# Kernel optimization log

Measured on AMD Instinct MI355X. Metric: run time of the kernel, lower is better.

The kernel has to match this reference:

```python
import jax, jax.numpy as jnp
import numpy as np
import math

NUM_HEADS = 8
QUERY_SIZE = 256
QK_SIZE = QUERY_SIZE // NUM_HEADS  # 32
VO_SIZE = QUERY_SIZE // NUM_HEADS  # 32
SEQ = 4096


def setup_inputs() -> dict:
    key = jax.random.key(0)
    kq, kk, kv, km, kwq, kwk, kwv, kwo = jax.random.split(key, 8)
    # equinox Linear weight shape is (out_features, in_features); y = W @ x
    lim_in = 1.0 / math.sqrt(QUERY_SIZE)
    lim_hd = 1.0 / math.sqrt(NUM_HEADS * VO_SIZE)
    return {
        "query": jax.random.normal(kq, (SEQ, QUERY_SIZE), dtype=jnp.float32),
        "key_": jax.random.normal(kk, (SEQ, QUERY_SIZE), dtype=jnp.float32),
        "value": jax.random.normal(kv, (SEQ, QUERY_SIZE), dtype=jnp.float32),
        "radial_mask": jax.random.uniform(km, (SEQ,), dtype=jnp.float32),
        "Wq": jax.random.uniform(kwq, (NUM_HEADS * QK_SIZE, QUERY_SIZE), minval=-lim_in, maxval=lim_in, dtype=jnp.float32),
        "Wk": jax.random.uniform(kwk, (NUM_HEADS * QK_SIZE, QUERY_SIZE), minval=-lim_in, maxval=lim_in, dtype=jnp.float32),
        "Wv": jax.random.uniform(kwv, (NUM_HEADS * VO_SIZE, QUERY_SIZE), minval=-lim_in, maxval=lim_in, dtype=jnp.float32),
        "Wo": jax.random.uniform(kwo, (QUERY_SIZE, NUM_HEADS * VO_SIZE), minval=-lim_hd, maxval=lim_hd, dtype=jnp.float32),
    }


def reference(query, key_, value, radial_mask, Wq, Wk, Wv, Wo):
    S = query.shape[0]
    # QKV projections, split into heads: [S, H, D]
    q = (query @ Wq.T).reshape(S, NUM_HEADS, QK_SIZE)
    k = (key_ @ Wk.T).reshape(S, NUM_HEADS, QK_SIZE)
    v = (value @ Wv.T).reshape(S, NUM_HEADS, VO_SIZE)
    # radial scaling of values (per kv position)
    v = radial_mask[:, None, None] * v
    # scaled dot-product attention per head; logits: [H, S, S]
    scale = 1.0 / math.sqrt(QK_SIZE)
    logits = jnp.einsum("shd,Shd->hsS", q * scale, k)
    weights = jax.nn.softmax(logits, axis=-1)
    attn = jnp.einsum("hsS,Shd->shd", weights, v).reshape(S, NUM_HEADS * VO_SIZE)
    # output projection
    return attn @ Wo.T
```

## Files before the change

kernel.cpp:

```cpp
#include <hip/hip_runtime.h>
#include <cstdint>

#define SEQ 4096
#define NH 8
#define DH 32

typedef __bf16 bf16x8 __attribute__((ext_vector_type(8)));
typedef float f32x4 __attribute__((ext_vector_type(4)));
typedef float f32x8 __attribute__((ext_vector_type(8)));
typedef float f32x16 __attribute__((ext_vector_type(16)));
typedef unsigned short u16x8 __attribute__((ext_vector_type(8)));
typedef unsigned u32x4 __attribute__((ext_vector_type(4)));
typedef unsigned u32x2 __attribute__((ext_vector_type(2)));
typedef int i32x2 __attribute__((ext_vector_type(2)));

#define MFMA16 __builtin_amdgcn_mfma_f32_16x16x32_bf16
#define MFMA32 __builtin_amdgcn_mfma_f32_32x32x16_bf16

#define QSCALE 0.25503902427f

__device__ inline bf16x8 ld_bf8(const unsigned short* p) {
    return __builtin_bit_cast(bf16x8, *(const u16x8*)p);
}
__device__ inline unsigned short bfbits(float v) {
    return __builtin_bit_cast(unsigned short, (__bf16)v);
}
__device__ inline bf16x8 cvt_f8(f32x8 v) {
    bf16x8 r;
#pragma unroll
    for (int i = 0; i < 8; i++) r[i] = (__bf16)v[i];
    return r;
}
__device__ inline unsigned cvtpk(float lo, float hi) {
    unsigned r;
    asm("v_cvt_pk_bf16_f32 %0, %1, %2" : "=v"(r) : "v"(lo), "v"(hi));
    return r;
}

__global__ __launch_bounds__(256) void precvt_kernel(
    const float* __restrict__ x0, const float* __restrict__ x1, const float* __restrict__ x2,
    const float* __restrict__ w0, const float* __restrict__ w1, const float* __restrict__ w2,
    const float* __restrict__ w3,
    unsigned short* __restrict__ bx0, unsigned short* __restrict__ bx1,
    unsigned short* __restrict__ bx2, unsigned short* __restrict__ bw0,
    unsigned short* __restrict__ bw1, unsigned short* __restrict__ bw2,
    unsigned short* __restrict__ bw3) {
    const int i = blockIdx.x * 256 + threadIdx.x;
    const float* src;
    unsigned short* dst;
    int off;
    float scale = 1.0f;
    if (i < 393216) {
        const int sel = i >> 17;
        off = i & 131071;
        src = (sel == 0) ? x0 : (sel == 1) ? x1 : x2;
        dst = (sel == 0) ? bx0 : (sel == 1) ? bx1 : bx2;
        if (sel == 0) scale = QSCALE;
    } else {
        const int j = i - 393216;
        const int sel = j >> 13;
        off = j & 8191;
        src = (sel == 0) ? w0 : (sel == 1) ? w1 : (sel == 2) ? w2 : w3;
        dst = (sel == 0) ? bw0 : (sel == 1) ? bw1 : (sel == 2) ? bw2 : bw3;
    }
    f32x8 v = ((const f32x8*)src)[off];
    u16x8 r;
#pragma unroll
    for (int j = 0; j < 8; j++) r[j] = bfbits(v[j] * scale);
    ((u16x8*)dst)[off] = r;
}

__global__ __launch_bounds__(256, 4) void proj_bf16_kernel(
    const unsigned short* __restrict__ X0, const unsigned short* __restrict__ X1,
    const unsigned short* __restrict__ X2, const unsigned short* __restrict__ W0,
    const unsigned short* __restrict__ W1, const unsigned short* __restrict__ W2,
    const float* __restrict__ radial,
    unsigned short* __restrict__ outq, unsigned short* __restrict__ outk,
    unsigned short* __restrict__ outv) {
    const int sel = blockIdx.y;
    const unsigned short* X = (sel == 0) ? X0 : (sel == 1) ? X1 : X2;
    const unsigned short* W = (sel == 0) ? W0 : (sel == 1) ? W1 : W2;
    const int lane = threadIdx.x & 63;
    const int w = threadIdx.x >> 6;
    const int cl = lane & 15;
    const int h4 = lane >> 4;
    const int t = blockIdx.x * 4 + w;
    const int m0 = (t >> 3) * 32;
    const int n0 = (t & 7) * 32;

    const unsigned short* xa0 = X + (m0 + cl) * 256 + h4 * 8;
    const unsigned short* xa1 = xa0 + 16 * 256;
    const unsigned short* wb0 = W + (n0 + cl) * 256 + h4 * 8;
    const unsigned short* wb1 = wb0 + 16 * 256;

    f32x4 acc00 = {0.f, 0.f, 0.f, 0.f}, acc01 = {0.f, 0.f, 0.f, 0.f};
    f32x4 acc10 = {0.f, 0.f, 0.f, 0.f}, acc11 = {0.f, 0.f, 0.f, 0.f};
#pragma unroll
    for (int ksi = 0; ksi < 8; ksi++) {
        bf16x8 a0 = ld_bf8(xa0 + ksi * 32);
        bf16x8 a1 = ld_bf8(xa1 + ksi * 32);
        bf16x8 b0 = ld_bf8(wb0 + ksi * 32);
        bf16x8 b1 = ld_bf8(wb1 + ksi * 32);
        acc00 = MFMA16(a0, b0, acc00, 0, 0, 0);
        acc01 = MFMA16(a0, b1, acc01, 0, 0, 0);
        acc10 = MFMA16(a1, b0, acc10, 0, 0, 0);
        acc11 = MFMA16(a1, b1, acc11, 0, 0, 0);
    }

#pragma unroll
    for (int am = 0; am < 2; am++) {
#pragma unroll
        for (int r = 0; r < 4; r++) {
            const int cm = m0 + am * 16 + h4 * 4 + r;
            float rm = (sel == 2) ? radial[cm] : 0.f;
#pragma unroll
            for (int bn = 0; bn < 2; bn++) {
                float v = am ? (bn ? acc11[r] : acc10[r]) : (bn ? acc01[r] : acc00[r]);
                const int cn = n0 + bn * 16 + cl;
                const int h = cn >> 5, d = cn & 31;
                if (sel == 0) outq[(h * SEQ + cm) * DH + d] = bfbits(v);
                else if (sel == 1) outk[(h * SEQ + cm) * DH + d] = bfbits(v);
                else outv[(h * DH + d) * SEQ + cm] = bfbits(v * rm);
            }
        }
    }
}

__global__ __launch_bounds__(256) void proj_f32_kernel(
    const float* __restrict__ X0, const float* __restrict__ X1, const float* __restrict__ X2,
    const float* __restrict__ W0, const float* __restrict__ W1, const float* __restrict__ W2,
    const float* __restrict__ radial,
    unsigned short* __restrict__ outq, unsigned short* __restrict__ outk,
    unsigned short* __restrict__ outv) {
    const int sel = blockIdx.y;
    const float* X = (sel == 0) ? X0 : (sel == 1) ? X1 : X2;
    const float* W = (sel == 0) ? W0 : (sel == 1) ? W1 : W2;
    const int lane = threadIdx.x & 63;
    const int w = threadIdx.x >> 6;
    const int cl = lane & 15;
    const int h4 = lane >> 4;
    const int t = blockIdx.x * 4 + w;
    const int m0 = (t >> 3) * 32;
    const int n0 = (t & 7) * 32;

    const float* xa0 = X + (m0 + cl) * 256 + h4 * 8;
    const float* xa1 = xa0 + 16 * 256;
    const float* wb0 = W + (n0 + cl) * 256 + h4 * 8;
    const float* wb1 = wb0 + 16 * 256;

    f32x4 acc00 = {0.f, 0.f, 0.f, 0.f}, acc01 = {0.f, 0.f, 0.f, 0.f};
    f32x4 acc10 = {0.f, 0.f, 0.f, 0.f}, acc11 = {0.f, 0.f, 0.f, 0.f};
#pragma unroll
    for (int ksi = 0; ksi < 8; ksi++) {
        bf16x8 a0 = cvt_f8(*(const f32x8*)(xa0 + ksi * 32));
        bf16x8 a1 = cvt_f8(*(const f32x8*)(xa1 + ksi * 32));
        bf16x8 b0 = cvt_f8(*(const f32x8*)(wb0 + ksi * 32));
        bf16x8 b1 = cvt_f8(*(const f32x8*)(wb1 + ksi * 32));
        acc00 = MFMA16(a0, b0, acc00, 0, 0, 0);
        acc01 = MFMA16(a0, b1, acc01, 0, 0, 0);
        acc10 = MFMA16(a1, b0, acc10, 0, 0, 0);
        acc11 = MFMA16(a1, b1, acc11, 0, 0, 0);
    }
#pragma unroll
    for (int am = 0; am < 2; am++) {
#pragma unroll
        for (int r = 0; r < 4; r++) {
            const int cm = m0 + am * 16 + h4 * 4 + r;
            float rm = (sel == 2) ? radial[cm] : 0.f;
#pragma unroll
            for (int bn = 0; bn < 2; bn++) {
                float v = am ? (bn ? acc11[r] : acc10[r]) : (bn ? acc01[r] : acc00[r]);
                const int cn = n0 + bn * 16 + cl;
                const int h = cn >> 5, d = cn & 31;
                if (sel == 0) outq[(h * SEQ + cm) * DH + d] = bfbits(v * QSCALE);
                else if (sel == 1) outk[(h * SEQ + cm) * DH + d] = bfbits(v);
                else outv[(h * DH + d) * SEQ + cm] = bfbits(v * rm);
            }
        }
    }
}

__device__ inline f32x16 qk_step(bf16x8 kf0, bf16x8 kf1, const bf16x8& qf0,
                                 const bf16x8& qf1) {
    f32x16 s = {0.f, 0.f, 0.f, 0.f, 0.f, 0.f, 0.f, 0.f,
                0.f, 0.f, 0.f, 0.f, 0.f, 0.f, 0.f, 0.f};
    __builtin_amdgcn_s_setprio(1);
    s = MFMA32(kf0, qf0, s, 0, 0, 0);
    s = MFMA32(kf1, qf1, s, 0, 0, 0);
    __builtin_amdgcn_s_setprio(0);
    return s;
}

__device__ inline void sm_pv_step(const f32x16& s, bf16x8 vt0, bf16x8 vt1,
                                  f32x16& oacc, float& ls) {
    float p[16];
#pragma unroll
    for (int r = 0; r < 16; r++) p[r] = __builtin_amdgcn_exp2f(s[r]);
    {
        float s01 = p[0] + p[1], s23 = p[2] + p[3], s45 = p[4] + p[5], s67 = p[6] + p[7];
        float s89 = p[8] + p[9], sab = p[10] + p[11], scd = p[12] + p[13], sef = p[14] + p[15];
        ls += ((s01 + s23) + (s45 + s67)) + ((s89 + sab) + (scd + sef));
    }
    unsigned a01 = cvtpk(p[0], p[1]), a23 = cvtpk(p[2], p[3]);
    unsigned a45 = cvtpk(p[4], p[5]), a67 = cvtpk(p[6], p[7]);
    i32x2 r0 = __builtin_amdgcn_permlane32_swap((int)a01, (int)a45, false, false);
    i32x2 r1 = __builtin_amdgcn_permlane32_swap((int)a23, (int)a67, false, false);
    u32x4 pb0w = {(unsigned)r0[0], (unsigned)r1[0], (unsigned)r0[1], (unsigned)r1[1]};
    unsigned a89 = cvtpk(p[8], p[9]), aab = cvtpk(p[10], p[11]);
    unsigned acd = cvtpk(p[12], p[13]), aef = cvtpk(p[14], p[15]);
    i32x2 r2 = __builtin_amdgcn_permlane32_swap((int)a89, (int)acd, false, false);
    i32x2 r3 = __builtin_amdgcn_permlane32_swap((int)aab, (int)aef, false, false);
    u32x4 pb1w = {(unsigned)r2[0], (unsigned)r3[0], (unsigned)r2[1], (unsigned)r3[1]};
    __builtin_amdgcn_s_setprio(1);
    oacc = MFMA32(vt0, __builtin_bit_cast(bf16x8, pb0w), oacc, 0, 0, 0);
    oacc = MFMA32(vt1, __builtin_bit_cast(bf16x8, pb1w), oacc, 0, 0, 0);
    __builtin_amdgcn_s_setprio(0);
}

__global__ __launch_bounds__(512, 2) void attn_kernel(
    const unsigned short* __restrict__ Q, const unsigned short* __restrict__ K,
    const unsigned short* __restrict__ Vt, unsigned short* __restrict__ An) {
    __shared__ float cO[7][64][16];
    __shared__ float cls[7][4][32];
    const int lane = threadIdx.x & 63;
    const int w = threadIdx.x >> 6;
    const int l31 = lane & 31;
    const int hi = lane >> 5;

    int bid = blockIdx.x;
    bid = (bid & 7) * 32 + (bid >> 3);
    const int head = bid >> 5;
    const int m0 = (bid & 31) * 128;

    const unsigned short* qh = Q + head * (SEQ * DH);
    const unsigned short* kh = K + head * (SEQ * DH);
    const unsigned short* vh = Vt + head * (DH * SEQ);

    bf16x8 q0[4], q1[4];
#pragma unroll
    for (int c = 0; c < 4; c++) {
        q0[c] = ld_bf8(qh + (m0 + c * 32 + l31) * DH + hi * 8);
        q1[c] = ld_bf8(qh + (m0 + c * 32 + l31) * DH + 16 + hi * 8);
    }

    f32x16 o[4];
    float ls[4];
#pragma unroll
    for (int c = 0; c < 4; c++) {
        o[c] = (f32x16){0.f, 0.f, 0.f, 0.f, 0.f, 0.f, 0.f, 0.f,
                        0.f, 0.f, 0.f, 0.f, 0.f, 0.f, 0.f, 0.f};
        ls[c] = 0.f;
    }

    const unsigned short* kp = kh + (w * 512 + l31) * DH + hi * 8;
    const unsigned short* vp = vh + l31 * SEQ + w * 512 + hi * 8;

    for (int nb = 0; nb < 16; nb++) {
        bf16x8 kc0 = ld_bf8(kp), kc1 = ld_bf8(kp + 16);
        bf16x8 vc0 = ld_bf8(vp), vc1 = ld_bf8(vp + 16);
#pragma unroll
        for (int c = 0; c < 4; c++) {
            f32x16 s = qk_step(kc0, kc1, q0[c], q1[c]);
            sm_pv_step(s, vc0, vc1, o[c], ls[c]);
        }
        kp += 32 * DH;
        vp += 32;
    }

#pragma unroll
    for (int c = 0; c < 4; c++) ls[c] += __shfl_xor(ls[c], 32);

#pragma unroll
    for (int c = 0; c < 4; c++) {
        if (w > 0) {
#pragma unroll
            for (int i = 0; i < 16; i++) cO[w - 1][lane][i] = o[c][i];
            if (hi == 0) cls[w - 1][c][l31] = ls[c];
        }
        __syncthreads();
        if (w == 0) {
#pragma unroll
            for (int j = 0; j < 7; j++) {
#pragma unroll
                for (int i = 0; i < 16; i++) o[c][i] += cO[j][lane][i];
            }
        }
        __syncthreads();
    }

    if (w == 0) {
#pragma unroll
        for (int c = 0; c < 4; c++) {
            float lt = ls[c];
#pragma unroll
            for (int j = 0; j < 7; j++) lt += cls[j][c][l31];
            const float inv = 1.0f / lt;
            unsigned short* op = An + (m0 + c * 32 + l31) * 256 + head * DH;
#pragma unroll
            for (int g = 0; g < 4; g++) {
                unsigned lo = cvtpk(o[c][4 * g] * inv, o[c][4 * g + 1] * inv);
                unsigned hw = cvtpk(o[c][4 * g + 2] * inv, o[c][4 * g + 3] * inv);
                *(u32x2*)(op + 8 * g + 4 * hi) = (u32x2){lo, hw};
            }
        }
    }
}

__global__ __launch_bounds__(256, 4) void oproj_bf16_kernel(
    const unsigned short* __restrict__ An, const unsigned short* __restrict__ Wo,
    float* __restrict__ out) {
    const int lane = threadIdx.x & 63;
    const int w = threadIdx.x >> 6;
    const int cl = lane & 15;
    const int h4 = lane >> 4;
    const int t = blockIdx.x * 4 + w;
    const int m0 = (t >> 4) * 32;
    const int n0 = (t & 15) * 16;

    const unsigned short* ap0 = An + (m0 + cl) * 256 + h4 * 8;
    const unsigned short* ap1 = ap0 + 16 * 256;
    const unsigned short* wb0 = Wo + (n0 + cl) * 256 + h4 * 8;

    f32x4 acc00 = {0.f, 0.f, 0.f, 0.f}, acc10 = {0.f, 0.f, 0.f, 0.f};
#pragma unroll
    for (int ksi = 0; ksi < 8; ksi++) {
        bf16x8 a0 = ld_bf8(ap0 + ksi * 32);
        bf16x8 a1 = ld_bf8(ap1 + ksi * 32);
        bf16x8 b0 = ld_bf8(wb0 + ksi * 32);
        acc00 = MFMA16(a0, b0, acc00, 0, 0, 0);
        acc10 = MFMA16(a1, b0, acc10, 0, 0, 0);
    }
#pragma unroll
    for (int am = 0; am < 2; am++) {
#pragma unroll
        for (int r = 0; r < 4; r++) {
            const int cm = m0 + am * 16 + h4 * 4 + r;
            out[cm * 256 + n0 + cl] = am ? acc10[r] : acc00[r];
        }
    }
}

__global__ __launch_bounds__(256) void oproj_f32_kernel(
    const unsigned short* __restrict__ An, const float* __restrict__ Wo,
    float* __restrict__ out) {
    const int lane = threadIdx.x & 63;
    const int w = threadIdx.x >> 6;
    const int cl = lane & 15;
    const int h4 = lane >> 4;
    const int t = blockIdx.x * 4 + w;
    const int m0 = (t >> 3) * 32;
    const int n0 = (t & 7) * 32;

    const unsigned short* ap0 = An + (m0 + cl) * 256 + h4 * 8;
    const unsigned short* ap1 = ap0 + 16 * 256;
    const float* wb0 = Wo + (n0 + cl) * 256 + h4 * 8;
    const float* wb1 = wb0 + 16 * 256;

    f32x4 acc00 = {0.f, 0.f, 0.f, 0.f}, acc01 = {0.f, 0.f, 0.f, 0.f};
    f32x4 acc10 = {0.f, 0.f, 0.f, 0.f}, acc11 = {0.f, 0.f, 0.f, 0.f};
#pragma unroll
    for (int ksi = 0; ksi < 8; ksi++) {
        bf16x8 a0 = ld_bf8(ap0 + ksi * 32);
        bf16x8 a1 = ld_bf8(ap1 + ksi * 32);
        bf16x8 b0 = cvt_f8(*(const f32x8*)(wb0 + ksi * 32));
        bf16x8 b1 = cvt_f8(*(const f32x8*)(wb1 + ksi * 32));
        acc00 = MFMA16(a0, b0, acc00, 0, 0, 0);
        acc01 = MFMA16(a0, b1, acc01, 0, 0, 0);
        acc10 = MFMA16(a1, b0, acc10, 0, 0, 0);
        acc11 = MFMA16(a1, b1, acc11, 0, 0, 0);
    }
#pragma unroll
    for (int am = 0; am < 2; am++) {
#pragma unroll
        for (int r = 0; r < 4; r++) {
            const int cm = m0 + am * 16 + h4 * 4 + r;
#pragma unroll
            for (int bn = 0; bn < 2; bn++) {
                float v = am ? (bn ? acc11[r] : acc10[r]) : (bn ? acc01[r] : acc00[r]);
                out[cm * 256 + n0 + bn * 16 + cl] = v;
            }
        }
    }
}

extern "C" void kernel_launch(void* const* d_in, const int* in_sizes, int n_in,
                              void* d_out, int out_size, void* d_ws, size_t ws_size,
                              hipStream_t stream) {
    const float* query = (const float*)d_in[0];
    const float* key_ = (const float*)d_in[1];
    const float* value = (const float*)d_in[2];
    const float* radial = (const float*)d_in[3];
    const float* Wq = (const float*)d_in[4];
    const float* Wk = (const float*)d_in[5];
    const float* Wv = (const float*)d_in[6];
    const float* Wo = (const float*)d_in[7];

    const size_t MB = 1u << 20;
    uint8_t* base = (uint8_t*)d_ws;
    unsigned short* wq = (unsigned short*)(base + 0 * MB);
    unsigned short* wk = (unsigned short*)(base + 2 * MB);
    unsigned short* wv = (unsigned short*)(base + 4 * MB);
    unsigned short* wa = (unsigned short*)(base + 6 * MB);

    if (ws_size >= (size_t)(15.5 * 1024 * 1024)) {
        unsigned short* bX0 = (unsigned short*)(base + 8 * MB);
        unsigned short* bX1 = (unsigned short*)(base + 10 * MB);
        unsigned short* bX2 = (unsigned short*)(base + 12 * MB);
        unsigned short* bWq = (unsigned short*)(base + 14 * MB);
        unsigned short* bWk = (unsigned short*)(base + 14 * MB + 128 * 1024);
        unsigned short* bWv = (unsigned short*)(base + 14 * MB + 256 * 1024);
        unsigned short* bWo = (unsigned short*)(base + 14 * MB + 384 * 1024);
        precvt_kernel<<<1664, 256, 0, stream>>>(query, key_, value, Wq, Wk, Wv, Wo,
                                                bX0, bX1, bX2, bWq, bWk, bWv, bWo);
        proj_bf16_kernel<<<dim3(256, 3), 256, 0, stream>>>(bX0, bX1, bX2, bWq, bWk, bWv,
                                                           radial, wq, wk, wv);
        attn_kernel<<<256, 512, 0, stream>>>(wq, wk, wv, wa);
        oproj_bf16_kernel<<<512, 256, 0, stream>>>(wa, bWo, (float*)d_out);
    } else {
        proj_f32_kernel<<<dim3(256, 3), 256, 0, stream>>>(query, key_, value, Wq, Wk, Wv,
                                                          radial, wq, wk, wv);
        attn_kernel<<<256, 512, 0, stream>>>(wq, wk, wv, wa);
        oproj_f32_kernel<<<256, 256, 0, stream>>>(wa, Wo, (float*)d_out);
    }
}
```

Before: 62.18 us.

## Swap MFMA operands for V projection to coalesce transposed stores; drop setprio

For the V projection, the MFMA operands are swapped so each lane's accumulator rows run along head dimension d and columns along sequence. Stores into the transposed Vt layout then write contiguous sequence positions across lanes instead of scattered 2-byte writes. The radial mask is loaded once per lane rather than per element. Separately, the s_setprio raise and lower around the MFMA pairs in the attention inner loop is removed, which changes wave scheduling priority and could help or hurt the overlap of matrix and softmax work.

New measurement: 61.67 us. No clear change (-0.8%).

```diff
diff --git a/kernel.cpp b/kernel.cpp
--- a/kernel.cpp
+++ b/kernel.cpp
@@ -95,32 +95,59 @@
 
     f32x4 acc00 = {0.f, 0.f, 0.f, 0.f}, acc01 = {0.f, 0.f, 0.f, 0.f};
     f32x4 acc10 = {0.f, 0.f, 0.f, 0.f}, acc11 = {0.f, 0.f, 0.f, 0.f};
-#pragma unroll
-    for (int ksi = 0; ksi < 8; ksi++) {
-        bf16x8 a0 = ld_bf8(xa0 + ksi * 32);
-        bf16x8 a1 = ld_bf8(xa1 + ksi * 32);
-        bf16x8 b0 = ld_bf8(wb0 + ksi * 32);
-        bf16x8 b1 = ld_bf8(wb1 + ksi * 32);
-        acc00 = MFMA16(a0, b0, acc00, 0, 0, 0);
-        acc01 = MFMA16(a0, b1, acc01, 0, 0, 0);
-        acc10 = MFMA16(a1, b0, acc10, 0, 0, 0);
-        acc11 = MFMA16(a1, b1, acc11, 0, 0, 0);
-    }
-
-#pragma unroll
-    for (int am = 0; am < 2; am++) {
-#pragma unroll
-        for (int r = 0; r < 4; r++) {
-            const int cm = m0 + am * 16 + h4 * 4 + r;
-            float rm = (sel == 2) ? radial[cm] : 0.f;
-#pragma unroll
-            for (int bn = 0; bn < 2; bn++) {
-                float v = am ? (bn ? acc11[r] : acc10[r]) : (bn ? acc01[r] : acc00[r]);
-                const int cn = n0 + bn * 16 + cl;
-                const int h = cn >> 5, d = cn & 31;
-                if (sel == 0) outq[(h * SEQ + cm) * DH + d] = bfbits(v);
-                else if (sel == 1) outk[(h * SEQ + cm) * DH + d] = bfbits(v);
-                else outv[(h * DH + d) * SEQ + cm] = bfbits(v * rm);
+
+    if (sel < 2) {
+#pragma unroll
+        for (int ksi = 0; ksi < 8; ksi++) {
+            bf16x8 a0 = ld_bf8(xa0 + ksi * 32);
+            bf16x8 a1 = ld_bf8(xa1 + ksi * 32);
+            bf16x8 b0 = ld_bf8(wb0 + ksi * 32);
+            bf16x8 b1 = ld_bf8(wb1 + ksi * 32);
+            acc00 = MFMA16(a0, b0, acc00, 0, 0, 0);
+            acc01 = MFMA16(a0, b1, acc01, 0, 0, 0);
+            acc10 = MFMA16(a1, b0, acc10, 0, 0, 0);
+            acc11 = MFMA16(a1, b1, acc11, 0, 0, 0);
+        }
+        unsigned short* out = (sel == 0) ? outq : outk;
+#pragma unroll
+        for (int am = 0; am < 2; am++) {
+#pragma unroll
+            for (int r = 0; r < 4; r++) {
+                const int cm = m0 + am * 16 + h4 * 4 + r;
+#pragma unroll
+                for (int bn = 0; bn < 2; bn++) {
+                    float v = am ? (bn ? acc11[r] : acc10[r]) : (bn ? acc01[r] : acc00[r]);
+                    const int cn = n0 + bn * 16 + cl;
+                    const int h = cn >> 5, d = cn & 31;
+                    out[(h * SEQ + cm) * DH + d] = bfbits(v);
+                }
+            }
+        }
+    } else {
+#pragma unroll
+        for (int ksi = 0; ksi < 8; ksi++) {
+            bf16x8 a0 = ld_bf8(xa0 + ksi * 32);
+            bf16x8 a1 = ld_bf8(xa1 + ksi * 32);
+            bf16x8 b0 = ld_bf8(wb0 + ksi * 32);
+            bf16x8 b1 = ld_bf8(wb1 + ksi * 32);
+            acc00 = MFMA16(b0, a0, acc00, 0, 0, 0);
+            acc01 = MFMA16(b0, a1, acc01, 0, 0, 0);
+            acc10 = MFMA16(b1, a0, acc10, 0, 0, 0);
+            acc11 = MFMA16(b1, a1, acc11, 0, 0, 0);
+        }
+        const int h = n0 >> 5;
+        const float rm0 = radial[m0 + cl];
+        const float rm1 = radial[m0 + 16 + cl];
+#pragma unroll
+        for (int wb = 0; wb < 2; wb++) {
+#pragma unroll
+            for (int r = 0; r < 4; r++) {
+                const int d = wb * 16 + h4 * 4 + r;
+                unsigned short* vrow = outv + (h * DH + d) * SEQ + m0;
+                float v0 = wb ? acc10[r] : acc00[r];
+                float v1 = wb ? acc11[r] : acc01[r];
+                vrow[cl] = bfbits(v0 * rm0);
+                vrow[16 + cl] = bfbits(v1 * rm1);
             }
         }
     }
@@ -150,31 +177,59 @@
 
     f32x4 acc00 = {0.f, 0.f, 0.f, 0.f}, acc01 = {0.f, 0.f, 0.f, 0.f};
     f32x4 acc10 = {0.f, 0.f, 0.f, 0.f}, acc11 = {0.f, 0.f, 0.f, 0.f};
-#pragma unroll
-    for (int ksi = 0; ksi < 8; ksi++) {
-        bf16x8 a0 = cvt_f8(*(const f32x8*)(xa0 + ksi * 32));
-        bf16x8 a1 = cvt_f8(*(const f32x8*)(xa1 + ksi * 32));
-        bf16x8 b0 = cvt_f8(*(const f32x8*)(wb0 + ksi * 32));
-        bf16x8 b1 = cvt_f8(*(const f32x8*)(wb1 + ksi * 32));
-        acc00 = MFMA16(a0, b0, acc00, 0, 0, 0);
-        acc01 = MFMA16(a0, b1, acc01, 0, 0, 0);
-        acc10 = MFMA16(a1, b0, acc10, 0, 0, 0);
-        acc11 = MFMA16(a1, b1, acc11, 0, 0, 0);
-    }
-#pragma unroll
-    for (int am = 0; am < 2; am++) {
-#pragma unroll
-        for (int r = 0; r < 4; r++) {
-            const int cm = m0 + am * 16 + h4 * 4 + r;
-            float rm = (sel == 2) ? radial[cm] : 0.f;
-#pragma unroll
-            for (int bn = 0; bn < 2; bn++) {
-                float v = am ? (bn ? acc11[r] : acc10[r]) : (bn ? acc01[r] : acc00[r]);
-                const int cn = n0 + bn * 16 + cl;
-                const int h = cn >> 5, d = cn & 31;
-                if (sel == 0) outq[(h * SEQ + cm) * DH + d] = bfbits(v * QSCALE);
-                else if (sel == 1) outk[(h * SEQ + cm) * DH + d] = bfbits(v);
-                else outv[(h * DH + d) * SEQ + cm] = bfbits(v * rm);
+    if (sel < 2) {
+#pragma unroll
+        for (int ksi = 0; ksi < 8; ksi++) {
+            bf16x8 a0 = cvt_f8(*(const f32x8*)(xa0 + ksi * 32));
+            bf16x8 a1 = cvt_f8(*(const f32x8*)(xa1 + ksi * 32));
+            bf16x8 b0 = cvt_f8(*(const f32x8*)(wb0 + ksi * 32));
+            bf16x8 b1 = cvt_f8(*(const f32x8*)(wb1 + ksi * 32));
+            acc00 = MFMA16(a0, b0, acc00, 0, 0, 0);
+            acc01 = MFMA16(a0, b1, acc01, 0, 0, 0);
+            acc10 = MFMA16(a1, b0, acc10, 0, 0, 0);
+            acc11 = MFMA16(a1, b1, acc11, 0, 0, 0);
+        }
+        const float qs = (sel == 0) ? QSCALE : 1.0f;
+        unsigned short* out = (sel == 0) ? outq : outk;
+#pragma unroll
+        for (int am = 0; am < 2; am++) {
+#pragma unroll
+            for (int r = 0; r < 4; r++) {
+                const int cm = m0 + am * 16 + h4 * 4 + r;
+#pragma unroll
+                for (int bn = 0; bn < 2; bn++) {
+                    float v = am ? (bn ? acc11[r] : acc10[r]) : (bn ? acc01[r] : acc00[r]);
+                    const int cn = n0 + bn * 16 + cl;
+                    const int h = cn >> 5, d = cn & 31;
+                    out[(h * SEQ + cm) * DH + d] = bfbits(v * qs);
+                }
+            }
+        }
+    } else {
+#pragma unroll
+        for (int ksi = 0; ksi < 8; ksi++) {
+            bf16x8 a0 = cvt_f8(*(const f32x8*)(xa0 + ksi * 32));
+            bf16x8 a1 = cvt_f8(*(const f32x8*)(xa1 + ksi * 32));
+            bf16x8 b0 = cvt_f8(*(const f32x8*)(wb0 + ksi * 32));
+            bf16x8 b1 = cvt_f8(*(const f32x8*)(wb1 + ksi * 32));
+            acc00 = MFMA16(b0, a0, acc00, 0, 0, 0);
+            acc01 = MFMA16(b0, a1, acc01, 0, 0, 0);
+            acc10 = MFMA16(b1, a0, acc10, 0, 0, 0);
+            acc11 = MFMA16(b1, a1, acc11, 0, 0, 0);
+        }
+        const int h = n0 >> 5;
+        const float rm0 = radial[m0 + cl];
+        const float rm1 = radial[m0 + 16 + cl];
+#pragma unroll
+        for (int wb = 0; wb < 2; wb++) {
+#pragma unroll
+            for (int r = 0; r < 4; r++) {
+                const int d = wb * 16 + h4 * 4 + r;
+                unsigned short* vrow = outv + (h * DH + d) * SEQ + m0;
+                float v0 = wb ? acc10[r] : acc00[r];
+                float v1 = wb ? acc11[r] : acc01[r];
+                vrow[cl] = bfbits(v0 * rm0);
+                vrow[16 + cl] = bfbits(v1 * rm1);
             }
         }
     }
@@ -184,10 +239,8 @@
                                  const bf16x8& qf1) {
     f32x16 s = {0.f, 0.f, 0.f, 0.f, 0.f, 0.f, 0.f, 0.f,
                 0.f, 0.f, 0.f, 0.f, 0.f, 0.f, 0.f, 0.f};
-    __builtin_amdgcn_s_setprio(1);
     s = MFMA32(kf0, qf0, s, 0, 0, 0);
     s = MFMA32(kf1, qf1, s, 0, 0, 0);
-    __builtin_amdgcn_s_setprio(0);
     return s;
 }
 
@@ -211,10 +264,8 @@
     i32x2 r2 = __builtin_amdgcn_permlane32_swap((int)a89, (int)acd, false, false);
     i32x2 r3 = __builtin_amdgcn_permlane32_swap((int)aab, (int)aef, false, false);
     u32x4 pb1w = {(unsigned)r2[0], (unsigned)r3[0], (unsigned)r2[1], (unsigned)r3[1]};
-    __builtin_amdgcn_s_setprio(1);
     oacc = MFMA32(vt0, __builtin_bit_cast(bf16x8, pb0w), oacc, 0, 0, 0);
     oacc = MFMA32(vt1, __builtin_bit_cast(bf16x8, pb1w), oacc, 0, 0, 0);
-    __builtin_amdgcn_s_setprio(0);
 }
 
 __global__ __launch_bounds__(512, 2) void attn_kernel(
```
